# Kernel optimization log

Measured on AMD Instinct MI355X. Metric: run time of the kernel, lower is better.

The kernel has to match this reference:

```python
import jax, jax.numpy as jnp
import numpy as np
import math

B, F, S, D, NH, L, DFF, M = 8, 48, 64, 512, 8, 4, 2048, 64
PERIOD = 30
NEG = -1e9
EPS = 1e-5

def _slopes(n):
    start = 2.0 ** (-2.0 ** -(math.log2(n) - 3))
    return np.array([start * (start ** i) for i in range(n)], dtype=np.float32)

def _biased_mask():  # (NH, F, F): causal mask + periodic ALiBi bias, alibi[i,j] = -((i-j)//period)
    i = np.arange(F)[:, None]; j = np.arange(F)[None, :]
    alibi = -((i - j) // PERIOD).astype(np.float32)
    return jnp.asarray(np.where(j <= i, _slopes(NH)[:, None, None] * alibi, NEG).astype(np.float32))

def _ppe():  # (F, D): periodic sinusoidal positional encoding (period 30)
    pos = np.arange(PERIOD, dtype=np.float32)[:, None]
    div = np.exp(np.arange(0, D, 2, dtype=np.float32) * (-math.log(10000.0) / D))
    pe = np.zeros((PERIOD, D), np.float32)
    pe[:, 0::2] = np.sin(pos * div)
    pe[:, 1::2] = np.cos(pos * div)
    return jnp.asarray(np.tile(pe, (F // PERIOD + 1, 1))[:F])

BIASED_MASK = _biased_mask()
PE = _ppe()
MEM_MASK = jnp.where(jnp.eye(F, dtype=bool), 0.0, NEG)  # enc_dec diagonal mask (frame i <-> content i)

def _ln(x, g, b):
    mu = x.mean(-1, keepdims=True)
    var = ((x - mu) ** 2).mean(-1, keepdims=True)
    return (x - mu) * jax.lax.rsqrt(var + EPS) * g + b

def _mha(q, k, v, in_w, in_b, out_w, out_b, nh, mask=None):
    Bq, Tq, d = q.shape
    Tk = k.shape[1]
    dh = d // nh
    wq, wk, wv = jnp.split(in_w, 3, axis=0)
    bq, bk, bv = jnp.split(in_b, 3, axis=0)
    qh = (q @ wq.T + bq).reshape(Bq, Tq, nh, dh).transpose(0, 2, 1, 3)
    kh = (k @ wk.T + bk).reshape(Bq, Tk, nh, dh).transpose(0, 2, 1, 3)
    vh = (v @ wv.T + bv).reshape(Bq, Tk, nh, dh).transpose(0, 2, 1, 3)
    s = jnp.einsum('bhqd,bhkd->bhqk', qh, kh) / jnp.sqrt(jnp.float32(dh))
    if mask is not None:
        s = s + mask
    o = jnp.einsum('bhqk,bhkd->bhqd', jax.nn.softmax(s, axis=-1), vh)
    return o.transpose(0, 2, 1, 3).reshape(Bq, Tq, d) @ out_w.T + out_b

def setup_inputs():
    key = jax.random.key(0)
    ks = iter(jax.random.split(key, 40))
    r = lambda *sh: jax.random.normal(next(ks), sh, jnp.float32) * 0.02
    return dict(
        content_code=jax.random.normal(next(ks), (B, F, D), jnp.float32),
        style_code=jax.random.normal(next(ks), (B, D), jnp.float32),
        style_hiddens=jax.random.normal(next(ks), (B, S, D), jnp.float32),
        init_state=jax.random.normal(next(ks), (B, M), jnp.float32),
        ca_in_w=r(3 * D, D), ca_in_b=r(3 * D), ca_out_w=r(D, D), ca_out_b=r(D),
        se_w=r(D, 2 * D), se_b=r(D),
        mm_w=r(D, M), mm_b=r(D),
        mmr_w=r(M, D), mmr_b=r(M),
        sa_in_w=r(L, 3 * D, D), sa_in_b=r(L, 3 * D), sa_out_w=r(L, D, D), sa_out_b=r(L, D),
        xa_in_w=r(L, 3 * D, D), xa_in_b=r(L, 3 * D), xa_out_w=r(L, D, D), xa_out_b=r(L, D),
        ff1_w=r(L, DFF, D), ff1_b=r(L, DFF), ff2_w=r(L, D, DFF), ff2_b=r(L, D),
        ln_g=jnp.ones((L, 3, D), jnp.float32), ln_b=jnp.zeros((L, 3, D), jnp.float32),
    )

def _forward(content_code, style_code, style_hiddens, init_state,
             ca_in_w, ca_in_b, ca_out_w, ca_out_b, se_w, se_b,
             mm_w, mm_b, mmr_w, mmr_b,
             sa_in_w, sa_in_b, sa_out_w, sa_out_b,
             xa_in_w, xa_in_b, xa_out_w, xa_out_b,
             ff1_w, ff1_b, ff2_w, ff2_b, ln_g, ln_b):
    style_emb_g = style_code[:, None, :]
    # 1-head cross-attn of each content frame against style hiddens; the torch code
    # computes this one query (frame) at a time, which is mathematically identical.
    sel = _mha(content_code, style_hiddens, style_hiddens,
               ca_in_w, ca_in_b, ca_out_w, ca_out_b, 1)  # (B, F, D)

    def emb_new(feat, i):  # style_emb_map(cat([feat, style_emb_l_i])) + global style
        return (jnp.concatenate([feat, sel[:, i:i + 1]], -1) @ se_w.T + se_b) + style_emb_g

    def decoder(x, mem):  # post-norm TransformerDecoder, relu FFN, eval (no dropout)
        T = x.shape[1]
        tgt = BIASED_MASK[None, :, :T, :T]
        mmask = MEM_MASK[:T][None, None]  # (1,1,T,F)
        for l in range(L):
            x = _ln(x + _mha(x, x, x, sa_in_w[l], sa_in_b[l], sa_out_w[l], sa_out_b[l], NH, tgt),
                    ln_g[l, 0], ln_b[l, 0])
            x = _ln(x + _mha(x, mem, mem, xa_in_w[l], xa_in_b[l], xa_out_w[l], xa_out_b[l], NH, mmask),
                    ln_g[l, 1], ln_b[l, 1])
            h = jax.nn.relu(x @ ff1_w[l].T + ff1_b[l]) @ ff2_w[l].T + ff2_b[l]
            x = _ln(x + h, ln_g[l, 2], ln_b[l, 2])
        return x

    dec_emb = emb_new((init_state @ mm_w.T + mm_b)[:, None], 0)  # (B,1,D)
    dec_out = None
    for i in range(F):
        dec_input = dec_emb + PE[:dec_emb.shape[1]]
        dec_out = decoder(dec_input, content_code) @ mmr_w.T + mmr_b  # (B, i+1, M)
        new = dec_out[:, -1:] @ mm_w.T + mm_b
        dec_emb = jnp.concatenate([dec_emb, emb_new(new, i)], axis=1)
    return dec_out, sel

def reference(content_code, style_code, style_hiddens, init_state,
              ca_in_w, ca_in_b, ca_out_w, ca_out_b, se_w, se_b,
              mm_w, mm_b, mmr_w, mmr_b,
              sa_in_w, sa_in_b, sa_out_w, sa_out_b,
              xa_in_w, xa_in_b, xa_out_w, xa_out_b,
              ff1_w, ff1_b, ff2_w, ff2_b, ln_g, ln_b):
    return _forward(content_code, style_code, style_hiddens, init_state,
                    ca_in_w, ca_in_b, ca_out_w, ca_out_b, se_w, se_b,
                    mm_w, mm_b, mmr_w, mmr_b,
                    sa_in_w, sa_in_b, sa_out_w, sa_out_b,
                    xa_in_w, xa_in_b, xa_out_w, xa_out_b,
                    ff1_w, ff1_b, ff2_w, ff2_b, ln_g, ln_b)
```

## Files before the change

kernel.cpp:

```cpp
#include <hip/hip_runtime.h>
#include <hip/hip_fp16.h>


typedef _Float16 h2 __attribute__((ext_vector_type(2)));
__device__ inline h2 u2h(unsigned u){ union{unsigned u; h2 h;} c; c.u=u; return c.h; }
#if __has_builtin(__builtin_amdgcn_fdot2)
__device__ inline float FDOT2(h2 a, h2 b, float c){ return __builtin_amdgcn_fdot2(a, b, c, false); }
#else
__device__ inline float FDOT2(h2 a, h2 b, float c){
  return fmaf((float)a.y, (float)b.y, fmaf((float)a.x, (float)b.x, c));
}
#endif

__device__ inline float aload(const float* p){
  return __hip_atomic_load(p, __ATOMIC_RELAXED, __HIP_MEMORY_SCOPE_AGENT);
}
__device__ inline void astore(float* p, float v){
  __hip_atomic_store(p, v, __ATOMIC_RELAXED, __HIP_MEMORY_SCOPE_AGENT);
}
__device__ inline unsigned aloadu(const unsigned* p){
  return __hip_atomic_load(p, __ATOMIC_RELAXED, __HIP_MEMORY_SCOPE_AGENT);
}
__device__ inline void astoreu(unsigned* p, unsigned v){
  __hip_atomic_store(p, v, __ATOMIC_RELAXED, __HIP_MEMORY_SCOPE_AGENT);
}

#define FD4(w,x) do{ a0=FDOT2(u2h((w).x),u2h((x).x),a0); a1=FDOT2(u2h((w).y),u2h((x).y),a1); \
                     a2=FDOT2(u2h((w).z),u2h((x).z),a2); a3=FDOT2(u2h((w).w),u2h((x).w),a3);}while(0)

__device__ inline float dot128s(const ushort* wrow, const ushort* xh){
  const uint4* w4=(const uint4*)wrow; const uint4* x4=(const uint4*)xh;
  float a0=0.f,a1=0.f,a2=0.f,a3=0.f;
  #pragma unroll
  for(int i=0;i<16;++i){ uint4 w=w4[i], x=x4[i]; FD4(w,x); }
  return (a0+a1)+(a2+a3);
}
__device__ inline float dot128p(const uint4 (&pw)[16], const ushort* xh){
  const uint4* x4=(const uint4*)xh;
  float a0=0.f,a1=0.f,a2=0.f,a3=0.f;
  #pragma unroll
  for(int i=0;i<16;++i){ uint4 w=pw[i], x=x4[i]; FD4(w,x); }
  return (a0+a1)+(a2+a3);
}
__device__ inline float dot128p8(const uint4 (&pw)[8], const ushort* wrow, const ushort* xh){
  const uint4* w4=(const uint4*)wrow; const uint4* x4=(const uint4*)xh;
  float a0=0.f,a1=0.f,a2=0.f,a3=0.f;
  #pragma unroll
  for(int i=0;i<8;++i){ uint4 w=pw[i], x=x4[i]; FD4(w,x); }
  #pragma unroll
  for(int i=8;i<16;++i){ uint4 w=w4[i], x=x4[i]; FD4(w,x); }
  return (a0+a1)+(a2+a3);
}
__device__ inline float dot32s(const ushort* wrow, const ushort* xh){
  const uint4* w4=(const uint4*)wrow; const uint4* x4=(const uint4*)xh;
  float a0=0.f,a1=0.f,a2=0.f,a3=0.f;
  #pragma unroll
  for(int i=0;i<4;++i){ uint4 w=w4[i], x=x4[i]; FD4(w,x); }
  return (a0+a1)+(a2+a3);
}
__device__ inline float dot_f32(const float* wrow, const float* x, int n){
  const float4* w4 = (const float4*)wrow;
  float a0=0.f,a1=0.f,a2=0.f,a3=0.f;
  #pragma unroll 4
  for (int i=0; i<(n>>2); ++i){
    float4 w = w4[i]; const float* xp = x + i*4;
    a0 = fmaf(w.x, xp[0], a0); a1 = fmaf(w.y, xp[1], a1);
    a2 = fmaf(w.z, xp[2], a2); a3 = fmaf(w.w, xp[3], a3);
  }
  return (a0+a1)+(a2+a3);
}
__device__ inline float dot64f_p8(const float4 (&pw)[8], const float* wrow, const float* x){
  const float4* w4=(const float4*)wrow;
  float a0=0.f,a1=0.f,a2=0.f,a3=0.f;
  #pragma unroll
  for(int i=0;i<8;++i){ float4 w=pw[i]; const float* xp=x+i*4;
    a0=fmaf(w.x,xp[0],a0); a1=fmaf(w.y,xp[1],a1); a2=fmaf(w.z,xp[2],a2); a3=fmaf(w.w,xp[3],a3);}
  #pragma unroll
  for(int i=8;i<16;++i){ float4 w=w4[i]; const float* xp=x+i*4;
    a0=fmaf(w.x,xp[0],a0); a1=fmaf(w.y,xp[1],a1); a2=fmaf(w.z,xp[2],a2); a3=fmaf(w.w,xp[3],a3);}
  return (a0+a1)+(a2+a3);
}

#define XSP(e) (((e)>>6)*68 + ((e)&63))
#define XHP(e) (((e)>>7)*136 + ((e)&127))

__global__ void k_transpose(const float* __restrict__ src, float* __restrict__ dst, int R, int C,
                            size_t sStr, size_t dStr){
  __shared__ float tile[32][33];
  int z = blockIdx.z;
  src += (size_t)z*sStr; dst += (size_t)z*dStr;
  int cb = blockIdx.x*32, rb = blockIdx.y*32;
  int tx = threadIdx.x, ty = threadIdx.y;
  for (int i=ty; i<32; i+=8) tile[i][tx] = src[(size_t)(rb+i)*C + cb+tx];
  __syncthreads();
  for (int i=ty; i<32; i+=8) dst[(size_t)(cb+i)*R + rb+tx] = tile[tx][i];
}

__global__ void k_castall(const float* __restrict__ s1, const float* __restrict__ s2,
                          const float* __restrict__ s3, const float* __restrict__ s4,
                          __half* __restrict__ d){
  const int N1=4*1536*512, N2=4*512*512, N3=4*2048*512, N4=4*512*2048;
  const int total = N1+N2+N3+N4;
  for (int i = blockIdx.x*256 + threadIdx.x; i < total; i += gridDim.x*256){
    float v;
    if (i < N1) v = s1[i];
    else if (i < N1+N2) v = s2[i-N1];
    else if (i < N1+N2+N3) v = s3[i-N1-N2];
    else v = s4[i-N1-N2-N3];
    d[i] = __float2half(v);
  }
}

__global__ void k_linear(const float* __restrict__ A, int lda,
                         const float* __restrict__ Wt, int ldw,
                         const float* __restrict__ bias,
                         float* __restrict__ C, int ldc,
                         int O, int Din,
                         size_t aStr, size_t wStr, size_t bStr, size_t cStr){
  __shared__ float xs[8*1024];
  __shared__ float red[4096];
  int tid = threadIdx.x;
  int r0 = blockIdx.y*8;
  int z = blockIdx.z;
  const float* Az = A + (size_t)z*aStr;
  const float* Wz = Wt + (size_t)z*wStr;
  const float* Bz = bias ? bias + (size_t)z*bStr : nullptr;
  float* Cz = C + (size_t)z*cStr;
  for (int idx=tid; idx<8*Din; idx+=256){
    int ri = idx / Din, d = idx - ri*Din;
    xs[idx] = Az[(size_t)(r0+ri)*lda + d];
  }
  __syncthreads();
  int op = tid & 63, kp = tid >> 6;
  int o = blockIdx.x*128 + op*2;
  int dq = Din >> 2;
  float a0[8] = {0,0,0,0,0,0,0,0}, a1[8] = {0,0,0,0,0,0,0,0};
  for (int d = kp*dq; d < kp*dq+dq; ++d){
    float2 w = *reinterpret_cast<const float2*>(&Wz[(size_t)d*ldw + o]);
    #pragma unroll
    for (int ri=0; ri<8; ++ri){ float x = xs[ri*Din+d]; a0[ri] += x*w.x; a1[ri] += x*w.y; }
  }
  #pragma unroll
  for (int ri=0; ri<8; ++ri){
    red[((kp*64+op)*8+ri)*2]   = a0[ri];
    red[((kp*64+op)*8+ri)*2+1] = a1[ri];
  }
  __syncthreads();
  for (int idx = tid; idx < 1024; idx += 256){
    int ri = idx >> 7, oc = idx & 127;
    int opp = oc >> 1, c = oc & 1;
    float v = red[((0*64+opp)*8+ri)*2 + c] + red[((1*64+opp)*8+ri)*2 + c]
            + red[((2*64+opp)*8+ri)*2 + c] + red[((3*64+opp)*8+ri)*2 + c];
    int oo = blockIdx.x*128 + oc;
    if (Bz) v += Bz[oo];
    Cz[(size_t)(r0+ri)*ldc + oo] = v;
  }
}

__global__ void k_pe(float* __restrict__ pe){
  int idx = blockIdx.x*256 + threadIdx.x;
  int t = idx >> 9, d = idx & 511;
  int p = t % 30;
  int i2 = d & ~1;
  float div = __expf(-(float)i2 * (9.210340371976184f/512.f));
  float ang = (float)p * div;
  pe[idx] = (d & 1) ? cosf(ang) : sinf(ang);
}

__global__ void k_sel_attn(const float* __restrict__ qh, const float* __restrict__ kh,
                           const float* __restrict__ vh, float* __restrict__ o){
  int bf = blockIdx.x;
  int b  = bf / 48;
  int tid = threadIdx.x;
  __shared__ float qs[512];
  __shared__ float ps[64];
  qs[tid] = qh[(size_t)bf*512 + tid];
  qs[tid+256] = qh[(size_t)bf*512 + tid + 256];
  __syncthreads();
  if (tid < 64){
    const float* kr = kh + (size_t)(b*64+tid)*512;
    float a = 0.f;
    for (int d=0; d<512; ++d) a += qs[d]*kr[d];
    ps[tid] = a * 0.04419417382415922f;
  }
  __syncthreads();
  if (tid == 0){
    float m = -1e30f;
    for (int j=0;j<64;++j) m = fmaxf(m, ps[j]);
    float s = 0.f;
    for (int j=0;j<64;++j){ float e = __expf(ps[j]-m); ps[j]=e; s+=e; }
    float iv = 1.f/s;
    for (int j=0;j<64;++j) ps[j] *= iv;
  }
  __syncthreads();
  float a0=0.f, a1=0.f;
  for (int j=0;j<64;++j){
    const float* vr = vh + (size_t)(b*64+j)*512;
    float pj = ps[j];
    a0 += pj*vr[tid]; a1 += pj*vr[tid+256];
  }
  o[(size_t)bf*512+tid] = a0;
  o[(size_t)bf*512+tid+256] = a1;
}

__global__ void k_cat_tail(const float* __restrict__ sel, float* __restrict__ cat){
  int idx = blockIdx.x*256 + threadIdx.x;
  int b = idx >> 9, d = idx & 511;
  cat[b*1024 + 512 + d] = sel[(size_t)(b*48)*512 + d];
}
__global__ void k_add_style(const float* __restrict__ embt, const float* __restrict__ style,
                            float* __restrict__ emb){
  int idx = blockIdx.x*256 + threadIdx.x;
  emb[idx] = embt[idx] + style[idx];
}

struct DP {
  unsigned* fl;
  float* z;
  float* emb;
  const ushort *Wqkv, *Wo, *Wf1, *Wf2;
  const float *xa_c, *pe;
  const float *sa_in_b, *sa_out_b, *ff1_b, *ff2_b;
  const float *mmr_w, *mmr_b, *mm_w, *mm_b, *se_w, *se_b;
  const float *ln_g, *ln_b, *style, *sel;
  float* dec_out;
};

#define ZT 49152

__launch_bounds__(512, 2)
__global__ void k_decode(DP p){
  const int tid = threadIdx.x;
  const int i = blockIdx.x;
  const int role = ((i & 7) << 1) | ((i >> 3) & 1);
  const int b = i >> 4;
  const int h = role >> 1, half = role & 1;
  const float slope = exp2f(-(float)(h+1));

  __shared__ float kc[4*48*65];
  __shared__ float vs[4*48*64];
  __shared__ float xsp[8*68];
  __shared__ float red[512];
  __shared__ float qs[64], ps[64], d64[64];
  __shared__ float nsp[8*68];
  __shared__ float selp[8*68];
  __shared__ float lnred[16];
  __shared__ __align__(16) __half xhp[4*136];
  __shared__ __align__(16) __half anh[64];
  __shared__ __align__(16) __half hsh[128];

  unsigned* flb = p.fl + (size_t)b*48*9*16;
  float* zb = p.z + (size_t)b*48*ZT;

  auto waitf = [&](int tt, int ss){
    const unsigned* f = flb + (size_t)(tt*9+ss)*16;
    if (tid == 0){
      for (;;){
        unsigned ok = 1u;
        #pragma unroll
        for (int k=0; k<16; ++k) ok &= aloadu(f + k);
        if (ok) break;
        __builtin_amdgcn_s_sleep(1);
      }
    }
    __syncthreads();
  };
  auto post = [&](int tt, int ss){
    __syncthreads();
    if (tid == 0)
      astoreu(flb + (size_t)(tt*9+ss)*16 + role, 1u);
  };
  auto lnorm = [&](float v, const float* g, const float* bb,
                   bool toXs, bool toXh)->float{
    float s = v, q = v*v;
    #pragma unroll
    for (int off=32; off>0; off>>=1){ s += __shfl_xor(s, off, 64); q += __shfl_xor(q, off, 64); }
    if ((tid & 63) == 0){ lnred[tid>>6] = s; lnred[8+(tid>>6)] = q; }
    __syncthreads();
    s = 0.f; q = 0.f;
    #pragma unroll
    for (int w=0; w<8; ++w){ s += lnred[w]; q += lnred[8+w]; }
    float mu = s * (1.f/512.f);
    float rs = rsqrtf(q*(1.f/512.f) - mu*mu + 1e-5f);
    float r = (v-mu)*rs*g[tid] + bb[tid];
    if (toXs) xsp[XSP(tid)] = r;
    if (toXh) xhp[XHP(tid)] = __float2half(r);
    __syncthreads();
    return r;
  };

  for (int t=0; t<48; ++t){
    float* ztb = zb + (size_t)t*ZT;
    for (int l=0; l<4; ++l){
      float* zA = ztb + l*4096;
      float* zB = ztb + 16384 + l*8192;

      const float* xac = p.xa_c + ((size_t)l*384 + b*48 + t)*512;
      float xa = xac[tid];
      if (l == 3) selp[XSP(tid)] = p.sel[((size_t)b*48+t)*512 + tid];

      uint4 wq[16];
      const ushort* wqbase = nullptr;
      if (tid < 384){
        int row = tid >> 1, piece = tid & 1;
        int sec = row >> 6, dch = row & 63;
        int wrow = sec*512 + h*64 + dch;
        wqbase = p.Wqkv + ((size_t)l*1536 + wrow)*512 + piece*256;
        const uint4* w4 = (const uint4*)wqbase;
        #pragma unroll
        for (int k=0; k<16; ++k) wq[k] = w4[k];
      }

      if (l == 0){
        float pe0 = p.pe[t*512+tid];
        float e;
        if (t > 0){ waitf(t-1, 8); e = aload(p.emb + ((size_t)t*8+b)*512 + tid); }
        else        e = aload(p.emb + ((size_t)t*8+b)*512 + tid);
        float x = e + pe0;
        xsp[XSP(tid)] = x; xhp[XHP(tid)] = __float2half(x);
        __syncthreads();
      } else {
        waitf(t, (l-1)*2+1);
        const float* zprev = ztb + 16384 + (l-1)*8192;
        float z = 0.f;
        #pragma unroll
        for (int r16=0; r16<16; ++r16) z += aload(zprev + r16*512 + tid);
        lnorm(z, p.ln_g + ((l-1)*3+2)*512, p.ln_b + ((l-1)*3+2)*512, true, true);
      }
      if (tid < 384){
        int row = tid >> 1, piece = tid & 1;
        int sec = row >> 6, dch = row & 63;
        int wrow = sec*512 + h*64 + dch;
        float acc = dot128p(wq, (const ushort*)(xhp + (2*piece)*136))
                  + dot128s((const ushort*)wqbase + 128,
                            (const ushort*)(xhp + (2*piece+1)*136));
        acc += __shfl_xor(acc, 1, 64);
        if (piece == 0){
          acc += p.sa_in_b[l*1536+wrow];
          if (sec == 0) qs[dch] = acc;
          else if (sec == 1) kc[(l*48+t)*65 + dch] = acc;
          else vs[(l*48+t)*64 + dch] = acc;
        }
      }
      __syncthreads();
      if (tid < 64){
        float sc = -1e30f;
        if (tid <= t){
          float a = 0.f;
          const float* kr = &kc[(l*48+tid)*65];
          #pragma unroll
          for (int d=0; d<64; ++d) a = fmaf(qs[d], kr[d], a);
          sc = a*0.125f - ((t-tid) >= 30 ? slope : 0.f);
        }
        float m = sc;
        #pragma unroll
        for (int off=32; off>0; off>>=1) m = fmaxf(m, __shfl_xor(m, off, 64));
        float e = (tid <= t) ? __expf(sc-m) : 0.f;
        float s = e;
        #pragma unroll
        for (int off=32; off>0; off>>=1) s += __shfl_xor(s, off, 64);
        ps[tid] = e / s;
      }
      __syncthreads();
      {
        int d = tid & 63, jq = tid >> 6;
        float a = 0.f;
        for (int j=jq*6; j<jq*6+6; ++j)
          if (j <= t) a = fmaf(ps[j], vs[(l*48+j)*64 + d], a);
        red[tid] = a;
      }
      __syncthreads();
      if (tid < 64){
        float a = red[tid]+red[64+tid]+red[128+tid]+red[192+tid]
                + red[256+tid]+red[320+tid]+red[384+tid]+red[448+tid];
        anh[tid] = __float2half(a);
      }
      __syncthreads();
      {
        int oi = tid >> 1, piece = tid & 1;
        int o = half*256 + oi;
        float acc = dot32s((const ushort*)(p.Wo + (((size_t)l*512+o)*512 + h*64) + piece*32),
                           (const ushort*)anh + piece*32);
        acc += __shfl_xor(acc, 1, 64);
        if (piece == 0){
          if (h == 0) acc += xsp[XSP(o)] + p.sa_out_b[l*512+o];
          astore(zA + role*256 + oi, acc);
        }
      }
      post(t, l*2);

      uint4 wf1[8], wf2[8];
      {
        int row = tid >> 2, piece = tid & 3;
        const uint4* w4 = (const uint4*)(p.Wf1 + ((size_t)l*2048 + role*128 + row)*512 + piece*128);
        #pragma unroll
        for (int k=0; k<8; ++k) wf1[k] = w4[k];
        const uint4* w42 = (const uint4*)(p.Wf2 + ((size_t)l*512 + tid)*2048 + role*128);
        #pragma unroll
        for (int k=0; k<8; ++k) wf2[k] = w42[k];
      }

      float r;
      {
        waitf(t, l*2);
        int hf = tid >> 8, cc = tid & 255;
        float z = 0.f;
        #pragma unroll
        for (int h8=0; h8<8; ++h8) z += aload(zA + ((h8<<1)|hf)*256 + cc);
        float w = lnorm(z, p.ln_g + (l*3)*512, p.ln_b + (l*3)*512, false, false);
        float u = w + xa;
        r = lnorm(u, p.ln_g + (l*3+1)*512, p.ln_b + (l*3+1)*512, false, true);
      }
      {
        int row = tid >> 2, piece = tid & 3;
        float a = dot128p8(wf1,
                           (const ushort*)(p.Wf1 + ((size_t)l*2048 + role*128 + row)*512 + piece*128),
                           (const ushort*)(xhp + piece*136));
        a += __shfl_xor(a, 1, 64);
        a += __shfl_xor(a, 2, 64);
        if (piece == 0)
          hsh[row] = __float2half(fmaxf(a + p.ff1_b[l*2048 + role*128 + row], 0.f));
      }
      __syncthreads();
      {
        float a0 = dot128p8(wf2,
                            (const ushort*)(p.Wf2 + ((size_t)l*512 + tid)*2048 + role*128),
                            (const ushort*)hsh);
        if (role == 0) a0 += r + p.ff2_b[l*512+tid];
        astore(zB + role*512 + tid, a0);
      }
      post(t, l*2+1);
    }

    float4 wm[8];
    {
      int o8 = tid >> 3, p8 = tid & 7;
      const float4* w4 = (const float4*)(p.mmr_w + (size_t)o8*512 + p8*64);
      #pragma unroll
      for (int k=0; k<8; ++k) wm[k] = w4[k];
    }
    {
      waitf(t, 7);
      const float* zB3 = ztb + 16384 + 3*8192;
      float z = 0.f;
      #pragma unroll
      for (int r16=0; r16<16; ++r16) z += aload(zB3 + r16*512 + tid);
      lnorm(z, p.ln_g + 11*512, p.ln_b + 11*512, true, false);
    }
    {
      int o8 = tid >> 3, p8 = tid & 7;
      float a = dot64f_p8(wm, p.mmr_w + (size_t)o8*512 + p8*64, xsp + p8*68);
      a += __shfl_xor(a, 1, 64);
      a += __shfl_xor(a, 2, 64);
      a += __shfl_xor(a, 4, 64);
      if (p8 == 0) d64[o8] = a + p.mmr_b[o8];
    }
    __syncthreads();
    if (role == 0 && tid < 64) p.dec_out[((size_t)b*48+t)*64 + tid] = d64[tid];
    nsp[XSP(tid)] = dot_f32(p.mm_w + (size_t)tid*64, d64, 64) + p.mm_b[tid];
    __syncthreads();
    {
      int o5 = tid >> 4, p16 = tid & 15;
      int o = role*32 + o5;
      const float* xsrc = (p16 < 8) ? (nsp + p16*68) : (selp + (p16-8)*68);
      float acc = dot_f32(p.se_w + (size_t)o*1024 + p16*64, xsrc, 64);
      acc += __shfl_xor(acc, 1, 64);
      acc += __shfl_xor(acc, 2, 64);
      acc += __shfl_xor(acc, 4, 64);
      acc += __shfl_xor(acc, 8, 64);
      if (p16 == 0){
        acc += p.se_b[o] + p.style[(size_t)b*512+o];
        astore(p.emb + ((size_t)(t+1)*8+b)*512 + o, acc);
      }
    }
    post(t, 8);
  }
}

extern "C" void kernel_launch(void* const* d_in, const int* in_sizes, int n_in,
                              void* d_out, int out_size, void* d_ws, size_t ws_size,
                              hipStream_t stream){
  (void)in_sizes; (void)n_in; (void)out_size; (void)ws_size;
  const float* content = (const float*)d_in[0];
  const float* style   = (const float*)d_in[1];
  const float* shid    = (const float*)d_in[2];
  const float* init_st = (const float*)d_in[3];
  const float* ca_in_w = (const float*)d_in[4];
  const float* ca_in_b = (const float*)d_in[5];
  const float* ca_out_w= (const float*)d_in[6];
  const float* ca_out_b= (const float*)d_in[7];
  const float* se_w    = (const float*)d_in[8];
  const float* se_b    = (const float*)d_in[9];
  const float* mm_w    = (const float*)d_in[10];
  const float* mm_b    = (const float*)d_in[11];
  const float* mmr_w   = (const float*)d_in[12];
  const float* mmr_b   = (const float*)d_in[13];
  const float* sa_in_w = (const float*)d_in[14];
  const float* sa_in_b = (const float*)d_in[15];
  const float* sa_out_w= (const float*)d_in[16];
  const float* sa_out_b= (const float*)d_in[17];
  const float* xa_in_w = (const float*)d_in[18];
  const float* xa_in_b = (const float*)d_in[19];
  const float* xa_out_w= (const float*)d_in[20];
  const float* xa_out_b= (const float*)d_in[21];
  const float* ff1_w   = (const float*)d_in[22];
  const float* ff1_b   = (const float*)d_in[23];
  const float* ff2_w   = (const float*)d_in[24];
  const float* ff2_b   = (const float*)d_in[25];
  const float* ln_g    = (const float*)d_in[26];
  const float* ln_b    = (const float*)d_in[27];

  float* out = (float*)d_out;
  float* dec_out = out;
  float* sel = out + 8*48*64;

  char* base = (char*)d_ws;
  size_t cur = 0;
  auto alloc = [&](size_t bytes)->char*{
    char* pt = base + cur;
    cur += (bytes + 255) & ~(size_t)255;
    return pt;
  };
  unsigned* fl  = (unsigned*)alloc((size_t)8*48*9*16*4);
  size_t zero_span = cur;
  float* zacc   = (float*)alloc((size_t)8*48*49152*4);
  float* emb    = (float*)alloc((size_t)49*8*512*4);
  ushort* WqkvH = (ushort*)alloc((size_t)4*1536*512*2);
  ushort* WoH   = (ushort*)alloc((size_t)4*512*512*2);
  ushort* Wf1H  = (ushort*)alloc((size_t)4*2048*512*2);
  ushort* Wf2H  = (ushort*)alloc((size_t)4*512*2048*2);
  float* Wt_mm    = (float*)alloc((size_t)64*512*4);
  float* Wt_se    = (float*)alloc((size_t)1024*512*4);
  float* Wt_ca_in = (float*)alloc((size_t)512*1536*4);
  float* Wt_ca_out= (float*)alloc((size_t)512*512*4);
  float* Wt_xa_v  = (float*)alloc((size_t)4*512*512*4);
  float* Wt_xa_o  = (float*)alloc((size_t)4*512*512*4);
  float* xa_c  = (float*)alloc((size_t)4*384*512*4);
  float* pe    = (float*)alloc((size_t)48*512*4);
  float* qh    = (float*)alloc((size_t)384*512*4);
  float* khb   = (float*)alloc((size_t)512*512*4);
  float* vhb   = (float*)alloc((size_t)512*512*4);
  float* attno = (float*)alloc((size_t)384*512*4);
  float* xtmp4 = (float*)alloc((size_t)4*384*512*4);
  float* catb  = (float*)alloc((size_t)8*1024*4);
  float* embt  = (float*)alloc((size_t)8*512*4);
  (void)vhb;

  hipMemsetAsync(fl, 0, zero_span, stream);

  dim3 tb(32,8);
  k_castall<<<4096, 256, 0, stream>>>(sa_in_w, sa_out_w, ff1_w, ff2_w, (__half*)WqkvH);
  k_transpose<<<dim3(16,16,4), tb, 0, stream>>>(xa_in_w + (size_t)1024*512, Wt_xa_v, 512, 512,
                                                (size_t)1536*512, (size_t)512*512);
  k_transpose<<<dim3(16,16,4), tb, 0, stream>>>(xa_out_w, Wt_xa_o, 512, 512,
                                                (size_t)512*512, (size_t)512*512);
  k_transpose<<<dim3(16,48), tb, 0, stream>>>(ca_in_w,  Wt_ca_in, 1536, 512, 0, 0);
  k_transpose<<<dim3(16,16), tb, 0, stream>>>(ca_out_w, Wt_ca_out, 512, 512, 0, 0);
  k_transpose<<<dim3(32,16), tb, 0, stream>>>(se_w,  Wt_se, 512, 1024, 0, 0);
  k_transpose<<<dim3(2,16),  tb, 0, stream>>>(mm_w,  Wt_mm, 512, 64, 0, 0);

  k_pe<<<96, 256, 0, stream>>>(pe);

  k_linear<<<dim3(4,48), 256, 0, stream>>>(content, 512, Wt_ca_in, 1536, ca_in_b, qh, 512, 512, 512, 0,0,0,0);
  k_linear<<<dim3(4,64,2), 256, 0, stream>>>(shid, 512, Wt_ca_in + 512, 1536, ca_in_b + 512, khb, 512, 512, 512,
                                             0, 512, 512, (size_t)512*512);
  k_sel_attn<<<384, 256, 0, stream>>>(qh, khb, vhb, attno);
  k_linear<<<dim3(4,48), 256, 0, stream>>>(attno, 512, Wt_ca_out, 512, ca_out_b, sel, 512, 512, 512, 0,0,0,0);

  k_linear<<<dim3(4,48,4), 256, 0, stream>>>(content, 512, Wt_xa_v, 512, xa_in_b + 1024, xtmp4, 512, 512, 512,
                                             0, (size_t)512*512, 1536, (size_t)384*512);
  k_linear<<<dim3(4,48,4), 256, 0, stream>>>(xtmp4, 512, Wt_xa_o, 512, xa_out_b, xa_c, 512, 512, 512,
                                             (size_t)384*512, (size_t)512*512, 512, (size_t)384*512);

  k_linear<<<dim3(4,1), 256, 0, stream>>>(init_st, 64, Wt_mm, 512, mm_b, catb, 1024, 512, 64, 0,0,0,0);
  k_cat_tail<<<16, 256, 0, stream>>>(sel, catb);
  k_linear<<<dim3(4,1), 256, 0, stream>>>(catb, 1024, Wt_se, 512, se_b, embt, 512, 512, 1024, 0,0,0,0);
  k_add_style<<<16, 256, 0, stream>>>(embt, style, emb);

  DP p;
  p.fl = fl; p.z = zacc; p.emb = emb;
  p.Wqkv = WqkvH; p.Wo = WoH; p.Wf1 = Wf1H; p.Wf2 = Wf2H;
  p.xa_c = xa_c; p.pe = pe;
  p.sa_in_b = sa_in_b; p.sa_out_b = sa_out_b; p.ff1_b = ff1_b; p.ff2_b = ff2_b;
  p.mmr_w = mmr_w; p.mmr_b = mmr_b; p.mm_w = mm_w; p.mm_b = mm_b;
  p.se_w = se_w; p.se_b = se_b; p.ln_g = ln_g; p.ln_b = ln_b;
  p.style = style; p.sel = sel; p.dec_out = dec_out;

  k_decode<<<dim3(128), dim3(512), 0, stream>>>(p);
}
```

Baseline: 5.792 ms.

## Reduce partial sums via global atomic adds instead of per-role slabs

Each of the 16 cooperating blocks per batch now atomically adds its partial output into one shared 512-float accumulator per stage, instead of writing its own slab that every consumer then sums with 8 or 16 loads. The flag wait is also parallelised: 16 threads each poll one flag rather than thread 0 looping over all 16. The aim is less cross-block reduction traffic and a smaller workspace, at the cost of atomic contention and a nondeterministic float summation order. The zeroed span now covers the accumulator and embedding buffers, so those are reset before each launch.

Result: faster. 5.172 ms (-10.7%).

```diff
diff --git a/kernel.cpp b/kernel.cpp
--- a/kernel.cpp
+++ b/kernel.cpp
@@ -226,8 +226,6 @@
   float* dec_out;
 };
 
-#define ZT 49152
-
 __launch_bounds__(512, 2)
 __global__ void k_decode(DP p){
   const int tid = threadIdx.x;
@@ -250,20 +248,16 @@
   __shared__ __align__(16) __half hsh[128];
 
   unsigned* flb = p.fl + (size_t)b*48*9*16;
-  float* zb = p.z + (size_t)b*48*ZT;
-
-  auto waitf = [&](int tt, int ss){
+  float* zb = p.z + (size_t)b*48*8*512;
+
+  auto waitz = [&](int tt, int ss, const float* src)->float{
     const unsigned* f = flb + (size_t)(tt*9+ss)*16;
-    if (tid == 0){
-      for (;;){
-        unsigned ok = 1u;
-        #pragma unroll
-        for (int k=0; k<16; ++k) ok &= aloadu(f + k);
-        if (ok) break;
+    if (tid < 16){
+      while (aloadu(f + tid) == 0u)
         __builtin_amdgcn_s_sleep(1);
-      }
     }
     __syncthreads();
+    return aload(src + tid);
   };
   auto post = [&](int tt, int ss){
     __syncthreads();
@@ -290,11 +284,7 @@
   };
 
   for (int t=0; t<48; ++t){
-    float* ztb = zb + (size_t)t*ZT;
     for (int l=0; l<4; ++l){
-      float* zA = ztb + l*4096;
-      float* zB = ztb + 16384 + l*8192;
-
       const float* xac = p.xa_c + ((size_t)l*384 + b*48 + t)*512;
       float xa = xac[tid];
       if (l == 3) selp[XSP(tid)] = p.sel[((size_t)b*48+t)*512 + tid];
@@ -314,17 +304,13 @@
       if (l == 0){
         float pe0 = p.pe[t*512+tid];
         float e;
-        if (t > 0){ waitf(t-1, 8); e = aload(p.emb + ((size_t)t*8+b)*512 + tid); }
-        else        e = aload(p.emb + ((size_t)t*8+b)*512 + tid);
+        if (t > 0) e = waitz(t-1, 8, p.emb + ((size_t)t*8+b)*512);
+        else       e = aload(p.emb + ((size_t)t*8+b)*512 + tid);
         float x = e + pe0;
         xsp[XSP(tid)] = x; xhp[XHP(tid)] = __float2half(x);
         __syncthreads();
       } else {
-        waitf(t, (l-1)*2+1);
-        const float* zprev = ztb + 16384 + (l-1)*8192;
-        float z = 0.f;
-        #pragma unroll
-        for (int r16=0; r16<16; ++r16) z += aload(zprev + r16*512 + tid);
+        float z = waitz(t, (l-1)*2+1, zb + ((size_t)t*8 + (l-1)*2+1)*512);
         lnorm(z, p.ln_g + ((l-1)*3+2)*512, p.ln_b + ((l-1)*3+2)*512, true, true);
       }
       if (tid < 384){
@@ -384,7 +370,7 @@
         acc += __shfl_xor(acc, 1, 64);
         if (piece == 0){
           if (h == 0) acc += xsp[XSP(o)] + p.sa_out_b[l*512+o];
-          astore(zA + role*256 + oi, acc);
+          unsafeAtomicAdd(zb + ((size_t)t*8 + l*2)*512 + o, acc);
         }
       }
       post(t, l*2);
@@ -402,11 +388,7 @@
 
       float r;
       {
-        waitf(t, l*2);
-        int hf = tid >> 8, cc = tid & 255;
-        float z = 0.f;
-        #pragma unroll
-        for (int h8=0; h8<8; ++h8) z += aload(zA + ((h8<<1)|hf)*256 + cc);
+        float z = waitz(t, l*2, zb + ((size_t)t*8 + l*2)*512);
         float w = lnorm(z, p.ln_g + (l*3)*512, p.ln_b + (l*3)*512, false, false);
         float u = w + xa;
         r = lnorm(u, p.ln_g + (l*3+1)*512, p.ln_b + (l*3+1)*512, false, true);
@@ -427,7 +409,7 @@
                             (const ushort*)(p.Wf2 + ((size_t)l*512 + tid)*2048 + role*128),
                             (const ushort*)hsh);
         if (role == 0) a0 += r + p.ff2_b[l*512+tid];
-        astore(zB + role*512 + tid, a0);
+        unsafeAtomicAdd(zb + ((size_t)t*8 + l*2+1)*512 + tid, a0);
       }
       post(t, l*2+1);
     }
@@ -440,11 +422,7 @@
       for (int k=0; k<8; ++k) wm[k] = w4[k];
     }
     {
-      waitf(t, 7);
-      const float* zB3 = ztb + 16384 + 3*8192;
-      float z = 0.f;
-      #pragma unroll
-      for (int r16=0; r16<16; ++r16) z += aload(zB3 + r16*512 + tid);
+      float z = waitz(t, 7, zb + ((size_t)t*8 + 7)*512);
       lnorm(z, p.ln_g + 11*512, p.ln_b + 11*512, true, false);
     }
     {
@@ -522,9 +500,9 @@
     return pt;
   };
   unsigned* fl  = (unsigned*)alloc((size_t)8*48*9*16*4);
+  float* zacc   = (float*)alloc((size_t)8*48*8*512*4);
+  float* emb    = (float*)alloc((size_t)49*8*512*4);
   size_t zero_span = cur;
-  float* zacc   = (float*)alloc((size_t)8*48*49152*4);
-  float* emb    = (float*)alloc((size_t)49*8*512*4);
   ushort* WqkvH = (ushort*)alloc((size_t)4*1536*512*2);
   ushort* WoH   = (ushort*)alloc((size_t)4*512*512*2);
   ushort* Wf1H  = (ushort*)alloc((size_t)4*2048*512*2);
```
